# Kernel optimization log

Hardware: AMD Instinct MI355X
Metric: run time of the kernel (lower is better)

Reference implementation:

```python
import jax, jax.numpy as jnp
import numpy as np

T, C, H, W = 16, 3, 512, 512
PS, PT = 7, 1
NQ = 262144


def setup_inputs() -> dict:
    key = jax.random.key(0)
    k1, k2, k3, k4 = jax.random.split(key, 4)
    vid2fill = jnp.zeros((T, C, H, W), jnp.float32)
    patches = jax.random.normal(k1, (NQ, PT, C, PS, PS), jnp.float32)
    # queryInds columns: (t, h, w) top-left corners, each kept in-bounds
    qt = jax.random.randint(k2, (NQ, 1), 0, T - PT + 1)
    qh = jax.random.randint(k3, (NQ, 1), 0, H - PS + 1)
    qw = jax.random.randint(k4, (NQ, 1), 0, W - PS + 1)
    queryInds = jnp.concatenate([qt, qh, qw], axis=1).astype(jnp.int32)
    return {"vid2fill": vid2fill, "patches": patches, "queryInds": queryInds}


def reference(vid2fill, patches, queryInds):
    # vid2fill: [T,C,H,W]; patches: [N,pt,C,ps,ps]; queryInds: [N,3] = (t,h,w)
    T_, C_, H_, W_ = vid2fill.shape
    N, pt, _, ps, _ = patches.shape
    ti = queryInds[:, 0, None] + jnp.arange(pt)  # [N,pt]
    hi = queryInds[:, 1, None] + jnp.arange(ps)  # [N,ps]
    wi = queryInds[:, 2, None] + jnp.arange(ps)  # [N,ps]
    # flat spatial-temporal index over (t,h,w): [N,pt,ps,ps]
    flat = (ti[:, :, None, None] * H_ + hi[:, None, :, None]) * W_ + wi[:, None, None, :]
    # channels-last flat video [T*H*W, C] for a single vectorized scatter-add
    vid_flat = vid2fill.transpose(0, 2, 3, 1).reshape(-1, C_)
    p = patches.transpose(0, 1, 3, 4, 2).reshape(-1, C_)  # [N*pt*ps*ps, C]
    out = vid_flat.at[flat.reshape(-1)].add(p)
    return out.reshape(T_, H_, W_, C_).transpose(0, 3, 1, 2)
```

## Files before the change

### kernel.cpp

```cpp
#include <hip/hip_runtime.h>

constexpr int T_ = 16, C_ = 3, H_ = 512, W_ = 512, PS_ = 7;
constexpr int PATCH_ELEMS = C_ * PS_ * PS_;
constexpr int TILE  = 32;
constexpr int HALO  = PS_ - 1;
constexpr int LTILE = TILE + HALO;
constexpr int LSTRIDE = 40;
constexpr int NTH = H_ / TILE, NTW = W_ / TILE;
constexpr int NBINS = T_ * NTH * NTW;
constexpr int LDS_PER_C  = LTILE * LSTRIDE;
constexpr int NPLANES = 6;
constexpr int ACC_FLOATS = NPLANES * LDS_PER_C;
constexpr int INTERIOR   = C_ * TILE * TILE;
constexpr int HALO_A = HALO * LTILE;
constexpr int HALO_B = TILE * HALO;
constexpr int HALO_PER_C    = HALO_A + HALO_B;
constexpr int HALO_PER_TILE = C_ * HALO_PER_C;
constexpr int CAP = 160;
constexpr int BTHR = 384;
constexpr int BAND = HALO * TILE + (TILE - HALO) * HALO;

constexpr size_t OFF_COUNTS = 0;
constexpr size_t OFF_LIST   = 16384;
constexpr size_t OFF_HALO   = OFF_LIST + (size_t)NBINS * CAP * 4;
constexpr size_t WS_NEEDED  = OFF_HALO + (size_t)NBINS * HALO_PER_TILE * 4;

__global__ void zero_counts_kernel(int* counts) {
    counts[blockIdx.x * 1024 + threadIdx.x] = 0;
}

__global__ void scatter_kernel(const int* __restrict__ q, int* __restrict__ counts,
                               int* __restrict__ list, int nq) {
    int n = blockIdx.x * 256 + threadIdx.x;
    if (n >= nq) return;
    int t = q[3 * n], h = q[3 * n + 1], w = q[3 * n + 2];
    int bin = (t * NTH + (h >> 5)) * NTW + (w >> 5);
    int pos = atomicAdd(counts + bin, 1);
    if (pos < CAP) list[bin * CAP + pos] = (n << 10) | ((h & 31) << 5) | (w & 31);
}

__global__ __launch_bounds__(BTHR, 6) void accum_kernel(
    const float* __restrict__ patches, const int* __restrict__ counts,
    const int* __restrict__ list, const float* __restrict__ vid,
    float* __restrict__ out, float* __restrict__ halo) {
    __shared__ float acc[ACC_FLOATS];
    __shared__ int recs[CAP];
    const int bin = blockIdx.x;
    const int t = bin >> 8;
    const int h0 = ((bin >> 4) & 15) * TILE, w0 = (bin & 15) * TILE;
    const int tid = threadIdx.x;
    const int lane = tid & 63, wid = tid >> 6;
    const int c = wid >> 1, k = wid & 1;

    for (int i = tid; i < ACC_FLOATS; i += BTHR) acc[i] = 0.f;
    int cnt = counts[bin];
    if (cnt > CAP) cnt = CAP;
    if (tid < cnt) recs[tid] = list[bin * CAP + tid];
    __syncthreads();

    {
        const bool act = lane < PS_ * PS_;
        const int loff = act ? (lane / PS_) * LSTRIDE + (lane % PS_) : 0;
        float* __restrict__ ac = acc + (k * 3 + c) * LDS_PER_C;
        const float* __restrict__ pc = patches + c * (PS_ * PS_);
        const int lo = (k * cnt) >> 1;
        const int hi = ((k + 1) * cnt) >> 1;

        float v0=0,v1=0,v2=0,v3=0,v4=0,v5=0,v6=0,v7=0;
        int o0=0,o1=0,o2=0,o3=0,o4=0,o5=0,o6=0,o7=0;
#define LDR(vv,oo,ii) { int rr = recs[(ii)]; \
        oo = ((rr >> 5) & 31) * LSTRIDE + (rr & 31) + loff; \
        vv = act ? pc[(unsigned)(rr >> 10) * (unsigned)PATCH_ELEMS + lane] : 0.f; }
        if (lo     < hi) LDR(v0,o0, lo)
        if (lo + 1 < hi) LDR(v1,o1, lo+1)
        if (lo + 2 < hi) LDR(v2,o2, lo+2)
        if (lo + 3 < hi) LDR(v3,o3, lo+3)
        if (lo + 4 < hi) LDR(v4,o4, lo+4)
        if (lo + 5 < hi) LDR(v5,o5, lo+5)
        if (lo + 6 < hi) LDR(v6,o6, lo+6)
        if (lo + 7 < hi) LDR(v7,o7, lo+7)
        for (int p = lo; p < hi; p += 8) {
            float x0=v0,x1=v1,x2=v2,x3=v3,x4=v4,x5=v5,x6=v6,x7=v7;
            int q0=o0,q1=o1,q2=o2,q3=o3,q4=o4,q5=o5,q6=o6,q7=o7;
            int qq = p + 8;
            if (qq     < hi) LDR(v0,o0, qq)
            if (qq + 1 < hi) LDR(v1,o1, qq+1)
            if (qq + 2 < hi) LDR(v2,o2, qq+2)
            if (qq + 3 < hi) LDR(v3,o3, qq+3)
            if (qq + 4 < hi) LDR(v4,o4, qq+4)
            if (qq + 5 < hi) LDR(v5,o5, qq+5)
            if (qq + 6 < hi) LDR(v6,o6, qq+6)
            if (qq + 7 < hi) LDR(v7,o7, qq+7)
            if (act) {
                ac[q0] += x0;
                if (p + 1 < hi) ac[q1] += x1;
                if (p + 2 < hi) ac[q2] += x2;
                if (p + 3 < hi) ac[q3] += x3;
                if (p + 4 < hi) ac[q4] += x4;
                if (p + 5 < hi) ac[q5] += x5;
                if (p + 6 < hi) ac[q6] += x6;
                if (p + 7 < hi) ac[q7] += x7;
            }
        }
#undef LDR
    }
    __syncthreads();

    const size_t obase = (size_t)t * C_ * H_ * W_;
    for (int i = tid; i < INTERIOR / 4; i += BTHR) {
        int cc = i >> 8, rem = i & 255, y = rem >> 3, x4 = rem & 7;
        size_t g = obase + (size_t)cc * (H_ * W_) + (size_t)(h0 + y) * W_ + (w0 + x4 * 4);
        const float4 vv = *reinterpret_cast<const float4*>(vid + g);
        const int ao = cc * LDS_PER_C + y * LSTRIDE + x4 * 4;
        const float4 aa = *reinterpret_cast<const float4*>(&acc[ao]);
        const float4 bb = *reinterpret_cast<const float4*>(&acc[ao + 3 * LDS_PER_C]);
        float4 r;
        r.x = vv.x + aa.x + bb.x; r.y = vv.y + aa.y + bb.y;
        r.z = vv.z + aa.z + bb.z; r.w = vv.w + aa.w + bb.w;
        *reinterpret_cast<float4*>(out + g) = r;
    }
    float* hp = halo + (size_t)bin * HALO_PER_TILE;
    for (int i = tid; i < HALO_PER_TILE; i += BTHR) {
        int cc = i / HALO_PER_C, r = i % HALO_PER_C;
        int y, x;
        if (r < HALO_A) { y = TILE + r / LTILE; x = r % LTILE; }
        else            { int r2 = r - HALO_A; y = r2 / HALO; x = TILE + r2 % HALO; }
        int ao = cc * LDS_PER_C + y * LSTRIDE + x;
        hp[i] = acc[ao] + acc[ao + 3 * LDS_PER_C];
    }
}

__global__ void halo_add_kernel(const float* __restrict__ halo,
                                float* __restrict__ out, int total) {
    int idx = blockIdx.x * 256 + threadIdx.x;
    if (idx >= total) return;
    int bin = idx / (C_ * BAND);
    int r = idx - bin * (C_ * BAND);
    int c = r / BAND;
    int s = r - c * BAND;
    int hm, wm;
    if (s < HALO * TILE) { hm = s >> 5; wm = s & 31; }
    else { int s2 = s - HALO * TILE; hm = HALO + s2 / HALO; wm = s2 - (s2 / HALO) * HALO; }
    int t = bin >> 8, i = (bin >> 4) & 15, j = bin & 15;
    bool top  = (hm < HALO) && (i > 0);
    bool left = (wm < HALO) && (j > 0);
    if (!(top || left)) return;
    float a = 0.f;
    if (top) {
        int tb = (t * NTH + (i - 1)) * NTW + j;
        a += halo[(size_t)tb * HALO_PER_TILE + c * HALO_PER_C + hm * LTILE + wm];
    }
    if (left) {
        int tb = (t * NTH + i) * NTW + (j - 1);
        a += halo[(size_t)tb * HALO_PER_TILE + c * HALO_PER_C + HALO_A + hm * HALO + wm];
    }
    if (top && left) {
        int tb = (t * NTH + (i - 1)) * NTW + (j - 1);
        a += halo[(size_t)tb * HALO_PER_TILE + c * HALO_PER_C + hm * LTILE + (TILE + wm)];
    }
    size_t g = (((size_t)t * C_ + c) * H_ + (i * TILE + hm)) * W_ + (j * TILE + wm);
    out[g] += a;
}

__global__ void scatter_add_kernel(const float* __restrict__ patches,
                                   const int* __restrict__ qinds,
                                   float* __restrict__ out, int total) {
    int tid = blockIdx.x * blockDim.x + threadIdx.x;
    if (tid >= total) return;
    int n = tid / PATCH_ELEMS;
    int r = tid - n * PATCH_ELEMS;
    int c = r / (PS_ * PS_);
    int rr = r - c * (PS_ * PS_);
    int ih = rr / PS_, iw = rr - ih * PS_;
    int t = qinds[n * 3 + 0], h = qinds[n * 3 + 1], w = qinds[n * 3 + 2];
    int out_idx = ((t * C_ + c) * H_ + (h + ih)) * W_ + (w + iw);
    atomicAdd(out + out_idx, patches[tid]);
}

extern "C" void kernel_launch(void* const* d_in, const int* in_sizes, int n_in,
                              void* d_out, int out_size, void* d_ws, size_t ws_size,
                              hipStream_t stream) {
    const float* vid     = (const float*)d_in[0];
    const float* patches = (const float*)d_in[1];
    const int*   qinds   = (const int*)d_in[2];
    float*       out     = (float*)d_out;
    const int nq = in_sizes[2] / 3;

    if (ws_size < WS_NEEDED) {
        hipMemcpyAsync(out, vid, (size_t)out_size * sizeof(float),
                       hipMemcpyDeviceToDevice, stream);
        int total = nq * PATCH_ELEMS;
        scatter_add_kernel<<<(total + 255) / 256, 256, 0, stream>>>(patches, qinds, out, total);
        return;
    }

    char* ws = (char*)d_ws;
    int*   counts = (int*)(ws + OFF_COUNTS);
    int*   list   = (int*)(ws + OFF_LIST);
    float* halo   = (float*)(ws + OFF_HALO);

    zero_counts_kernel<<<NBINS / 1024, 1024, 0, stream>>>(counts);
    scatter_kernel<<<(nq + 255) / 256, 256, 0, stream>>>(qinds, counts, list, nq);
    accum_kernel<<<NBINS, BTHR, 0, stream>>>(patches, counts, list, vid, out, halo);
    int total_band = NBINS * C_ * BAND;
    halo_add_kernel<<<(total_band + 255) / 256, 256, 0, stream>>>(halo, out, total_band);
}
```

Before: 325.3 us.

## Stage patch loads into LDS via async global_load_lds with double buffering

```diff
diff --git a/kernel.cpp b/kernel.cpp
--- a/kernel.cpp
+++ b/kernel.cpp
@@ -9,21 +9,25 @@
 constexpr int NTH = H_ / TILE, NTW = W_ / TILE;
 constexpr int NBINS = T_ * NTH * NTW;
 constexpr int LDS_PER_C  = LTILE * LSTRIDE;
-constexpr int NPLANES = 6;
-constexpr int ACC_FLOATS = NPLANES * LDS_PER_C;
+constexpr int ACC_FLOATS = C_ * LDS_PER_C;
 constexpr int INTERIOR   = C_ * TILE * TILE;
 constexpr int HALO_A = HALO * LTILE;
 constexpr int HALO_B = TILE * HALO;
 constexpr int HALO_PER_C    = HALO_A + HALO_B;
 constexpr int HALO_PER_TILE = C_ * HALO_PER_C;
 constexpr int CAP = 160;
-constexpr int BTHR = 384;
+constexpr int BTHR = 192;
+constexpr int BR = 8;
+constexpr int SSLOT = 50;
 constexpr int BAND = HALO * TILE + (TILE - HALO) * HALO;
 
 constexpr size_t OFF_COUNTS = 0;
 constexpr size_t OFF_LIST   = 16384;
 constexpr size_t OFF_HALO   = OFF_LIST + (size_t)NBINS * CAP * 4;
 constexpr size_t WS_NEEDED  = OFF_HALO + (size_t)NBINS * HALO_PER_TILE * 4;
+
+typedef const __attribute__((address_space(1))) float* gas_fp;
+typedef __attribute__((address_space(3))) float* las_fp;
 
 __global__ void zero_counts_kernel(int* counts) {
     counts[blockIdx.x * 1024 + threadIdx.x] = 0;
@@ -39,18 +43,18 @@
     if (pos < CAP) list[bin * CAP + pos] = (n << 10) | ((h & 31) << 5) | (w & 31);
 }
 
-__global__ __launch_bounds__(BTHR, 6) void accum_kernel(
+__global__ __launch_bounds__(BTHR, 4) void accum_kernel(
     const float* __restrict__ patches, const int* __restrict__ counts,
     const int* __restrict__ list, const float* __restrict__ vid,
     float* __restrict__ out, float* __restrict__ halo) {
     __shared__ float acc[ACC_FLOATS];
+    __shared__ float stage[C_][2][BR * SSLOT];
     __shared__ int recs[CAP];
     const int bin = blockIdx.x;
     const int t = bin >> 8;
     const int h0 = ((bin >> 4) & 15) * TILE, w0 = (bin & 15) * TILE;
     const int tid = threadIdx.x;
     const int lane = tid & 63, wid = tid >> 6;
-    const int c = wid >> 1, k = wid & 1;
 
     for (int i = tid; i < ACC_FLOATS; i += BTHR) acc[i] = 0.f;
     int cnt = counts[bin];
@@ -59,50 +63,48 @@
     __syncthreads();
 
     {
+        const int c = wid;
         const bool act = lane < PS_ * PS_;
         const int loff = act ? (lane / PS_) * LSTRIDE + (lane % PS_) : 0;
-        float* __restrict__ ac = acc + (k * 3 + c) * LDS_PER_C;
-        const float* __restrict__ pc = patches + c * (PS_ * PS_);
-        const int lo = (k * cnt) >> 1;
-        const int hi = ((k + 1) * cnt) >> 1;
-
-        float v0=0,v1=0,v2=0,v3=0,v4=0,v5=0,v6=0,v7=0;
-        int o0=0,o1=0,o2=0,o3=0,o4=0,o5=0,o6=0,o7=0;
-#define LDR(vv,oo,ii) { int rr = recs[(ii)]; \
-        oo = ((rr >> 5) & 31) * LSTRIDE + (rr & 31) + loff; \
-        vv = act ? pc[(unsigned)(rr >> 10) * (unsigned)PATCH_ELEMS + lane] : 0.f; }
-        if (lo     < hi) LDR(v0,o0, lo)
-        if (lo + 1 < hi) LDR(v1,o1, lo+1)
-        if (lo + 2 < hi) LDR(v2,o2, lo+2)
-        if (lo + 3 < hi) LDR(v3,o3, lo+3)
-        if (lo + 4 < hi) LDR(v4,o4, lo+4)
-        if (lo + 5 < hi) LDR(v5,o5, lo+5)
-        if (lo + 6 < hi) LDR(v6,o6, lo+6)
-        if (lo + 7 < hi) LDR(v7,o7, lo+7)
-        for (int p = lo; p < hi; p += 8) {
-            float x0=v0,x1=v1,x2=v2,x3=v3,x4=v4,x5=v5,x6=v6,x7=v7;
-            int q0=o0,q1=o1,q2=o2,q3=o3,q4=o4,q5=o5,q6=o6,q7=o7;
-            int qq = p + 8;
-            if (qq     < hi) LDR(v0,o0, qq)
-            if (qq + 1 < hi) LDR(v1,o1, qq+1)
-            if (qq + 2 < hi) LDR(v2,o2, qq+2)
-            if (qq + 3 < hi) LDR(v3,o3, qq+3)
-            if (qq + 4 < hi) LDR(v4,o4, qq+4)
-            if (qq + 5 < hi) LDR(v5,o5, qq+5)
-            if (qq + 6 < hi) LDR(v6,o6, qq+6)
-            if (qq + 7 < hi) LDR(v7,o7, qq+7)
+        float* __restrict__ ac = acc + c * LDS_PER_C;
+        const int nb = (cnt + BR - 1) / BR;
+
+        auto issue = [&](int bb, int u) {
+            int base = bb * BR;
             if (act) {
-                ac[q0] += x0;
-                if (p + 1 < hi) ac[q1] += x1;
-                if (p + 2 < hi) ac[q2] += x2;
-                if (p + 3 < hi) ac[q3] += x3;
-                if (p + 4 < hi) ac[q4] += x4;
-                if (p + 5 < hi) ac[q5] += x5;
-                if (p + 6 < hi) ac[q6] += x6;
-                if (p + 7 < hi) ac[q7] += x7;
+#pragma unroll
+                for (int j = 0; j < BR; ++j) {
+                    int idx = base + j;
+                    if (idx > cnt - 1) idx = cnt - 1;
+                    int rr = recs[idx];
+                    const float* g = patches + (size_t)(unsigned)(rr >> 10) * PATCH_ELEMS
+                                     + c * (PS_ * PS_) + lane;
+                    __builtin_amdgcn_global_load_lds(
+                        (gas_fp)(const void*)g,
+                        (las_fp)(void*)&stage[c][u][j * SSLOT], 4, 0, 0);
+                }
+            }
+            __builtin_amdgcn_sched_barrier(0);
+        };
+
+        if (nb > 0) {
+            issue(0, 0);
+            issue(nb > 1 ? 1 : 0, 1);
+            for (int b = 0; b < nb; ++b) {
+                asm volatile("s_waitcnt vmcnt(8)" ::: "memory");
+                __builtin_amdgcn_sched_barrier(0);
+                const int base = b * BR;
+                int lim = cnt - base; if (lim > BR) lim = BR;
+                const float* sb = &stage[c][b & 1][0];
+                for (int j = 0; j < lim; ++j) {
+                    int rr = recs[base + j];
+                    int bofs = ((rr >> 5) & 31) * LSTRIDE + (rr & 31) + loff;
+                    if (act) ac[bofs] += sb[j * SSLOT + lane];
+                }
+                int nxt = b + 2; if (nxt > nb - 1) nxt = nb - 1;
+                issue(nxt, b & 1);
             }
         }
-#undef LDR
     }
     __syncthreads();
 
@@ -111,12 +113,9 @@
         int cc = i >> 8, rem = i & 255, y = rem >> 3, x4 = rem & 7;
         size_t g = obase + (size_t)cc * (H_ * W_) + (size_t)(h0 + y) * W_ + (w0 + x4 * 4);
         const float4 vv = *reinterpret_cast<const float4*>(vid + g);
-        const int ao = cc * LDS_PER_C + y * LSTRIDE + x4 * 4;
-        const float4 aa = *reinterpret_cast<const float4*>(&acc[ao]);
-        const float4 bb = *reinterpret_cast<const float4*>(&acc[ao + 3 * LDS_PER_C]);
-        float4 r;
-        r.x = vv.x + aa.x + bb.x; r.y = vv.y + aa.y + bb.y;
-        r.z = vv.z + aa.z + bb.z; r.w = vv.w + aa.w + bb.w;
+        const float4 aa = *reinterpret_cast<const float4*>(
+            &acc[cc * LDS_PER_C + y * LSTRIDE + x4 * 4]);
+        float4 r; r.x = vv.x + aa.x; r.y = vv.y + aa.y; r.z = vv.z + aa.z; r.w = vv.w + aa.w;
         *reinterpret_cast<float4*>(out + g) = r;
     }
     float* hp = halo + (size_t)bin * HALO_PER_TILE;
@@ -125,8 +124,7 @@
         int y, x;
         if (r < HALO_A) { y = TILE + r / LTILE; x = r % LTILE; }
         else            { int r2 = r - HALO_A; y = r2 / HALO; x = TILE + r2 % HALO; }
-        int ao = cc * LDS_PER_C + y * LSTRIDE + x;
-        hp[i] = acc[ao] + acc[ao + 3 * LDS_PER_C];
+        hp[i] = acc[cc * LDS_PER_C + y * LSTRIDE + x];
     }
 }
 
```

Result: no change. 330.5 us (+1.6%).

## Replace halo buffer pass with device copy plus atomic halo edges

Applied to the files above, without the earlier changes.

```diff
diff --git a/kernel.cpp b/kernel.cpp
--- a/kernel.cpp
+++ b/kernel.cpp
@@ -9,21 +9,16 @@
 constexpr int NTH = H_ / TILE, NTW = W_ / TILE;
 constexpr int NBINS = T_ * NTH * NTW;
 constexpr int LDS_PER_C  = LTILE * LSTRIDE;
-constexpr int NPLANES = 6;
-constexpr int ACC_FLOATS = NPLANES * LDS_PER_C;
-constexpr int INTERIOR   = C_ * TILE * TILE;
-constexpr int HALO_A = HALO * LTILE;
-constexpr int HALO_B = TILE * HALO;
-constexpr int HALO_PER_C    = HALO_A + HALO_B;
-constexpr int HALO_PER_TILE = C_ * HALO_PER_C;
+constexpr int ACC_FLOATS = C_ * LDS_PER_C;
 constexpr int CAP = 160;
-constexpr int BTHR = 384;
-constexpr int BAND = HALO * TILE + (TILE - HALO) * HALO;
+constexpr int BTHR = 192;
+constexpr int CSTR = 16;
+constexpr int NEX = 26 * 26;
+constexpr int NSH = 192 + 156 + 420;
 
 constexpr size_t OFF_COUNTS = 0;
-constexpr size_t OFF_LIST   = 16384;
-constexpr size_t OFF_HALO   = OFF_LIST + (size_t)NBINS * CAP * 4;
-constexpr size_t WS_NEEDED  = OFF_HALO + (size_t)NBINS * HALO_PER_TILE * 4;
+constexpr size_t OFF_LIST   = (size_t)NBINS * CSTR * 4;
+constexpr size_t WS_NEEDED  = OFF_LIST + (size_t)NBINS * CAP * 4;
 
 __global__ void zero_counts_kernel(int* counts) {
     counts[blockIdx.x * 1024 + threadIdx.x] = 0;
@@ -35,14 +30,13 @@
     if (n >= nq) return;
     int t = q[3 * n], h = q[3 * n + 1], w = q[3 * n + 2];
     int bin = (t * NTH + (h >> 5)) * NTW + (w >> 5);
-    int pos = atomicAdd(counts + bin, 1);
+    int pos = atomicAdd(counts + bin * CSTR, 1);
     if (pos < CAP) list[bin * CAP + pos] = (n << 10) | ((h & 31) << 5) | (w & 31);
 }
 
 __global__ __launch_bounds__(BTHR, 6) void accum_kernel(
     const float* __restrict__ patches, const int* __restrict__ counts,
-    const int* __restrict__ list, const float* __restrict__ vid,
-    float* __restrict__ out, float* __restrict__ halo) {
+    const int* __restrict__ list, float* __restrict__ out) {
     __shared__ float acc[ACC_FLOATS];
     __shared__ int recs[CAP];
     const int bin = blockIdx.x;
@@ -50,56 +44,54 @@
     const int h0 = ((bin >> 4) & 15) * TILE, w0 = (bin & 15) * TILE;
     const int tid = threadIdx.x;
     const int lane = tid & 63, wid = tid >> 6;
-    const int c = wid >> 1, k = wid & 1;
 
     for (int i = tid; i < ACC_FLOATS; i += BTHR) acc[i] = 0.f;
-    int cnt = counts[bin];
+    int cnt = counts[bin * CSTR];
     if (cnt > CAP) cnt = CAP;
     if (tid < cnt) recs[tid] = list[bin * CAP + tid];
     __syncthreads();
 
     {
+        const int c = wid;
         const bool act = lane < PS_ * PS_;
         const int loff = act ? (lane / PS_) * LSTRIDE + (lane % PS_) : 0;
-        float* __restrict__ ac = acc + (k * 3 + c) * LDS_PER_C;
+        float* __restrict__ ac = acc + c * LDS_PER_C;
         const float* __restrict__ pc = patches + c * (PS_ * PS_);
-        const int lo = (k * cnt) >> 1;
-        const int hi = ((k + 1) * cnt) >> 1;
 
         float v0=0,v1=0,v2=0,v3=0,v4=0,v5=0,v6=0,v7=0;
         int o0=0,o1=0,o2=0,o3=0,o4=0,o5=0,o6=0,o7=0;
 #define LDR(vv,oo,ii) { int rr = recs[(ii)]; \
         oo = ((rr >> 5) & 31) * LSTRIDE + (rr & 31) + loff; \
-        vv = act ? pc[(unsigned)(rr >> 10) * (unsigned)PATCH_ELEMS + lane] : 0.f; }
-        if (lo     < hi) LDR(v0,o0, lo)
-        if (lo + 1 < hi) LDR(v1,o1, lo+1)
-        if (lo + 2 < hi) LDR(v2,o2, lo+2)
-        if (lo + 3 < hi) LDR(v3,o3, lo+3)
-        if (lo + 4 < hi) LDR(v4,o4, lo+4)
-        if (lo + 5 < hi) LDR(v5,o5, lo+5)
-        if (lo + 6 < hi) LDR(v6,o6, lo+6)
-        if (lo + 7 < hi) LDR(v7,o7, lo+7)
-        for (int p = lo; p < hi; p += 8) {
+        vv = act ? pc[(size_t)(unsigned)(rr >> 10) * PATCH_ELEMS + lane] : 0.f; }
+        if (0 < cnt) LDR(v0,o0, 0)
+        if (1 < cnt) LDR(v1,o1, 1)
+        if (2 < cnt) LDR(v2,o2, 2)
+        if (3 < cnt) LDR(v3,o3, 3)
+        if (4 < cnt) LDR(v4,o4, 4)
+        if (5 < cnt) LDR(v5,o5, 5)
+        if (6 < cnt) LDR(v6,o6, 6)
+        if (7 < cnt) LDR(v7,o7, 7)
+        for (int p = 0; p < cnt; p += 8) {
             float x0=v0,x1=v1,x2=v2,x3=v3,x4=v4,x5=v5,x6=v6,x7=v7;
             int q0=o0,q1=o1,q2=o2,q3=o3,q4=o4,q5=o5,q6=o6,q7=o7;
             int qq = p + 8;
-            if (qq     < hi) LDR(v0,o0, qq)
-            if (qq + 1 < hi) LDR(v1,o1, qq+1)
-            if (qq + 2 < hi) LDR(v2,o2, qq+2)
-            if (qq + 3 < hi) LDR(v3,o3, qq+3)
-            if (qq + 4 < hi) LDR(v4,o4, qq+4)
-            if (qq + 5 < hi) LDR(v5,o5, qq+5)
-            if (qq + 6 < hi) LDR(v6,o6, qq+6)
-            if (qq + 7 < hi) LDR(v7,o7, qq+7)
+            if (qq     < cnt) LDR(v0,o0, qq)
+            if (qq + 1 < cnt) LDR(v1,o1, qq+1)
+            if (qq + 2 < cnt) LDR(v2,o2, qq+2)
+            if (qq + 3 < cnt) LDR(v3,o3, qq+3)
+            if (qq + 4 < cnt) LDR(v4,o4, qq+4)
+            if (qq + 5 < cnt) LDR(v5,o5, qq+5)
+            if (qq + 6 < cnt) LDR(v6,o6, qq+6)
+            if (qq + 7 < cnt) LDR(v7,o7, qq+7)
             if (act) {
                 ac[q0] += x0;
-                if (p + 1 < hi) ac[q1] += x1;
-                if (p + 2 < hi) ac[q2] += x2;
-                if (p + 3 < hi) ac[q3] += x3;
-                if (p + 4 < hi) ac[q4] += x4;
-                if (p + 5 < hi) ac[q5] += x5;
-                if (p + 6 < hi) ac[q6] += x6;
-                if (p + 7 < hi) ac[q7] += x7;
+                if (p + 1 < cnt) ac[q1] += x1;
+                if (p + 2 < cnt) ac[q2] += x2;
+                if (p + 3 < cnt) ac[q3] += x3;
+                if (p + 4 < cnt) ac[q4] += x4;
+                if (p + 5 < cnt) ac[q5] += x5;
+                if (p + 6 < cnt) ac[q6] += x6;
+                if (p + 7 < cnt) ac[q7] += x7;
             }
         }
 #undef LDR
@@ -107,59 +99,28 @@
     __syncthreads();
 
     const size_t obase = (size_t)t * C_ * H_ * W_;
-    for (int i = tid; i < INTERIOR / 4; i += BTHR) {
-        int cc = i >> 8, rem = i & 255, y = rem >> 3, x4 = rem & 7;
-        size_t g = obase + (size_t)cc * (H_ * W_) + (size_t)(h0 + y) * W_ + (w0 + x4 * 4);
-        const float4 vv = *reinterpret_cast<const float4*>(vid + g);
-        const int ao = cc * LDS_PER_C + y * LSTRIDE + x4 * 4;
-        const float4 aa = *reinterpret_cast<const float4*>(&acc[ao]);
-        const float4 bb = *reinterpret_cast<const float4*>(&acc[ao + 3 * LDS_PER_C]);
-        float4 r;
-        r.x = vv.x + aa.x + bb.x; r.y = vv.y + aa.y + bb.y;
-        r.z = vv.z + aa.z + bb.z; r.w = vv.w + aa.w + bb.w;
-        *reinterpret_cast<float4*>(out + g) = r;
+    for (int k = tid; k < C_ * NEX; k += BTHR) {
+        int c = k / NEX, r = k % NEX;
+        int y = 6 + r / 26, x = 6 + r % 26;
+        size_t g = obase + (size_t)c * (H_ * W_) + (size_t)(h0 + y) * W_ + (w0 + x);
+        out[g] += acc[c * LDS_PER_C + y * LSTRIDE + x];
     }
-    float* hp = halo + (size_t)bin * HALO_PER_TILE;
-    for (int i = tid; i < HALO_PER_TILE; i += BTHR) {
-        int cc = i / HALO_PER_C, r = i % HALO_PER_C;
+    for (int k = tid; k < C_ * NSH; k += BTHR) {
+        int c = k / NSH, r = k % NSH;
         int y, x;
-        if (r < HALO_A) { y = TILE + r / LTILE; x = r % LTILE; }
-        else            { int r2 = r - HALO_A; y = r2 / HALO; x = TILE + r2 % HALO; }
-        int ao = cc * LDS_PER_C + y * LSTRIDE + x;
-        hp[i] = acc[ao] + acc[ao + 3 * LDS_PER_C];
+        if (r < 192)      { y = r >> 5; x = r & 31; }
+        else if (r < 348) { int r2 = r - 192; y = 6 + r2 / 6; x = r2 % 6; }
+        else {
+            int r2 = r - 348;
+            if (r2 < 228) { y = TILE + r2 / LTILE; x = r2 % LTILE; }
+            else          { int r3 = r2 - 228; y = r3 / HALO; x = TILE + r3 % HALO; }
+        }
+        float v = acc[c * LDS_PER_C + y * LSTRIDE + x];
+        if (v != 0.f) {
+            size_t g = obase + (size_t)c * (H_ * W_) + (size_t)(h0 + y) * W_ + (w0 + x);
+            atomicAdd(out + g, v);
+        }
     }
-}
-
-__global__ void halo_add_kernel(const float* __restrict__ halo,
-                                float* __restrict__ out, int total) {
-    int idx = blockIdx.x * 256 + threadIdx.x;
-    if (idx >= total) return;
-    int bin = idx / (C_ * BAND);
-    int r = idx - bin * (C_ * BAND);
-    int c = r / BAND;
-    int s = r - c * BAND;
-    int hm, wm;
-    if (s < HALO * TILE) { hm = s >> 5; wm = s & 31; }
-    else { int s2 = s - HALO * TILE; hm = HALO + s2 / HALO; wm = s2 - (s2 / HALO) * HALO; }
-    int t = bin >> 8, i = (bin >> 4) & 15, j = bin & 15;
-    bool top  = (hm < HALO) && (i > 0);
-    bool left = (wm < HALO) && (j > 0);
-    if (!(top || left)) return;
-    float a = 0.f;
-    if (top) {
-        int tb = (t * NTH + (i - 1)) * NTW + j;
-        a += halo[(size_t)tb * HALO_PER_TILE + c * HALO_PER_C + hm * LTILE + wm];
-    }
-    if (left) {
-        int tb = (t * NTH + i) * NTW + (j - 1);
-        a += halo[(size_t)tb * HALO_PER_TILE + c * HALO_PER_C + HALO_A + hm * HALO + wm];
-    }
-    if (top && left) {
-        int tb = (t * NTH + (i - 1)) * NTW + (j - 1);
-        a += halo[(size_t)tb * HALO_PER_TILE + c * HALO_PER_C + hm * LTILE + (TILE + wm)];
-    }
-    size_t g = (((size_t)t * C_ + c) * H_ + (i * TILE + hm)) * W_ + (j * TILE + wm);
-    out[g] += a;
 }
 
 __global__ void scatter_add_kernel(const float* __restrict__ patches,
@@ -186,22 +147,20 @@
     float*       out     = (float*)d_out;
     const int nq = in_sizes[2] / 3;
 
+    hipMemcpyAsync(out, vid, (size_t)out_size * sizeof(float),
+                   hipMemcpyDeviceToDevice, stream);
+
     if (ws_size < WS_NEEDED) {
-        hipMemcpyAsync(out, vid, (size_t)out_size * sizeof(float),
-                       hipMemcpyDeviceToDevice, stream);
         int total = nq * PATCH_ELEMS;
         scatter_add_kernel<<<(total + 255) / 256, 256, 0, stream>>>(patches, qinds, out, total);
         return;
     }
 
     char* ws = (char*)d_ws;
-    int*   counts = (int*)(ws + OFF_COUNTS);
-    int*   list   = (int*)(ws + OFF_LIST);
-    float* halo   = (float*)(ws + OFF_HALO);
+    int* counts = (int*)(ws + OFF_COUNTS);
+    int* list   = (int*)(ws + OFF_LIST);
 
-    zero_counts_kernel<<<NBINS / 1024, 1024, 0, stream>>>(counts);
+    zero_counts_kernel<<<NBINS * CSTR / 1024, 1024, 0, stream>>>(counts);
     scatter_kernel<<<(nq + 255) / 256, 256, 0, stream>>>(qinds, counts, list, nq);
-    accum_kernel<<<NBINS, BTHR, 0, stream>>>(patches, counts, list, vid, out, halo);
-    int total_band = NBINS * C_ * BAND;
-    halo_add_kernel<<<(total_band + 255) / 256, 256, 0, stream>>>(halo, out, total_band);
+    accum_kernel<<<NBINS, BTHR, 0, stream>>>(patches, counts, list, out);
 }
```

Result: slower. 342.3 us (+5.2%).
